# Kernel tuning notes

Measured on AMD Instinct MI355X. Metric: run time of the kernel, lower is better.

## Reference

```python
import jax, jax.numpy as jnp
import numpy as np

H = 16
D_K = 64
HALF_WINDOW = 256  # window_size // 2 = 512 // 2


def setup_inputs() -> dict:
    key = jax.random.key(0)
    ks = jax.random.split(key, 9)
    B, S, D = 2, 2048, 1024
    scale = 0.02
    return {
        "x": jax.random.normal(ks[0], (B, S, D), dtype=jnp.float32),
        "Wq": jax.random.normal(ks[1], (D, D), dtype=jnp.float32) * scale,
        "bq": jax.random.normal(ks[2], (D,), dtype=jnp.float32) * scale,
        "Wk": jax.random.normal(ks[3], (D, D), dtype=jnp.float32) * scale,
        "bk": jax.random.normal(ks[4], (D,), dtype=jnp.float32) * scale,
        "Wv": jax.random.normal(ks[5], (D, D), dtype=jnp.float32) * scale,
        "bv": jax.random.normal(ks[6], (D,), dtype=jnp.float32) * scale,
        "Wo": jax.random.normal(ks[7], (D, D), dtype=jnp.float32) * scale,
        "bo": jax.random.normal(ks[8], (D,), dtype=jnp.float32) * scale,
    }


def reference(x, Wq, bq, Wk, bk, Wv, bv, Wo, bo):
    B, S, D = x.shape
    # projections -> [B, H, S, d_k]
    q = (x @ Wq + bq).reshape(B, S, H, D_K).transpose(0, 2, 1, 3)
    k = (x @ Wk + bk).reshape(B, S, H, D_K).transpose(0, 2, 1, 3)
    v = (x @ Wv + bv).reshape(B, S, H, D_K).transpose(0, 2, 1, 3)
    # dense scores, as in the original module
    scores = jnp.einsum("bhqd,bhkd->bhqk", q, k) / jnp.sqrt(jnp.float32(D_K))
    # sliding window band mask: 0 inside |i-j| <= half_window, -inf outside
    idx = jnp.arange(S)
    band = jnp.abs(idx[:, None] - idx[None, :]) <= HALF_WINDOW  # [S, S]
    window_mask = jnp.where(band, jnp.float32(0.0), -jnp.inf)
    scores = scores + window_mask[None, None, :, :]
    attn = jax.nn.softmax(scores, axis=-1)  # dropout is identity (p=0 / eval)
    out = jnp.einsum("bhqk,bhkd->bhqd", attn, v)  # [B, H, S, d_k]
    out = out.transpose(0, 2, 1, 3).reshape(B, S, D)
    return out @ Wo + bo
```

## Files before the change

### kernel.cpp

```cpp
#include <hip/hip_runtime.h>
#include <hip/hip_bf16.h>
#include <cstdint>
#include <cstddef>

using bf16 = __hip_bfloat16;
typedef __attribute__((ext_vector_type(8))) short bf16x8v;
typedef __attribute__((ext_vector_type(4))) float f32x4v;
typedef __attribute__((ext_vector_type(16))) float f32x16v;
typedef __attribute__((ext_vector_type(4))) int i32x4v;

__device__ __forceinline__ f32x4v mfma16x16x32(bf16x8v a, bf16x8v b, f32x4v c) {
  return __builtin_amdgcn_mfma_f32_16x16x32_bf16(a, b, c, 0, 0, 0);
}
__device__ __forceinline__ f32x16v mfma32x32x16(bf16x8v a, bf16x8v b, f32x16v c) {
  return __builtin_amdgcn_mfma_f32_32x32x16_bf16(a, b, c, 0, 0, 0);
}

__device__ __forceinline__ void lds_async16(const void* g, void* l) {
  __builtin_amdgcn_global_load_lds(
      (__attribute__((address_space(1))) void*)g,
      (__attribute__((address_space(3))) void*)l, 16, 0, 0);
}

__device__ __forceinline__ unsigned short f2bf_bits(float f) {
  union { bf16 h; unsigned short u; } cv;
  cv.h = __float2bfloat16(f);
  return cv.u;
}
__device__ __forceinline__ uint32_t pk_bf2(float a, float b) {
  return (uint32_t)f2bf_bits(a) | ((uint32_t)f2bf_bits(b) << 16);
}

#define QSC 0.18033688011111793f


__global__ void convert_x_k(const float* __restrict__ x, bf16* __restrict__ xb) {
  const int i = blockIdx.x * blockDim.x + threadIdx.x;
  const float4 v = reinterpret_cast<const float4*>(x)[i];
  ushort4 o;
  o.x = f2bf_bits(v.x); o.y = f2bf_bits(v.y);
  o.z = f2bf_bits(v.z); o.w = f2bf_bits(v.w);
  reinterpret_cast<ushort4*>(xb)[i] = o;
}

__global__ void transpose_w_k(const float* __restrict__ Wq, const float* __restrict__ Wk,
                              const float* __restrict__ Wv, const float* __restrict__ Wo,
                              bf16* __restrict__ wcat, bf16* __restrict__ wot) {
  __shared__ float tile[64][65];
  const int mat = blockIdx.z;
  const float* W = (mat == 0) ? Wq : (mat == 1) ? Wk : (mat == 2) ? Wv : Wo;
  bf16* dst = (mat < 3) ? (wcat + (size_t)mat * 1024 * 1024) : wot;
  const int n0 = blockIdx.x * 64, k0 = blockIdx.y * 64;
  const int tr = threadIdx.x >> 6, tc = threadIdx.x & 63;
#pragma unroll
  for (int it = 0; it < 16; ++it)
    tile[it * 4 + tr][tc] = W[(size_t)(k0 + it * 4 + tr) * 1024 + n0 + tc];
  __syncthreads();
#pragma unroll
  for (int it = 0; it < 16; ++it) {
    const int n = n0 + it * 4 + tr;
    dst[(size_t)n * 1024 + k0 + tc] = __float2bfloat16(tile[tc][it * 4 + tr]);
  }
}

__global__ void build_bias_k(const float* __restrict__ bq, const float* __restrict__ bk,
                             const float* __restrict__ bv, float* __restrict__ bcat) {
  const int i = blockIdx.x * 256 + threadIdx.x;
  if (i < 3072)
    bcat[i] = (i < 1024) ? bq[i] : (i < 2048) ? bk[i - 1024] : bv[i - 2048];
}

template <int EPI>
__global__ __launch_bounds__(256, 3) void gemm_k(
    const bf16* __restrict__ A, const bf16* __restrict__ Bt,
    const float* __restrict__ bias,
    bf16* __restrict__ qb, bf16* __restrict__ kb, bf16* __restrict__ vtb,
    float* __restrict__ outf)
{
  constexpr int K = 1024;
  __shared__ bf16 smem[16384];
  const int t = threadIdx.x;
  const int lane = t & 63, w = t >> 6;
  const int g = lane >> 4, r = lane & 15;
  const int wr = w >> 1, wc = w & 1;
  const int m0 = blockIdx.x * 128, n0 = blockIdx.y * 128;

  const int srow = t >> 2;
  const int scol = ((lane & 3) ^ g) << 3;
  const bf16* aS0 = A + (size_t)(m0 + srow) * K + scol;
  const bf16* aS1 = A + (size_t)(m0 + 64 + srow) * K + scol;
  const bf16* bS0 = Bt + (size_t)(n0 + srow) * K + scol;
  const bf16* bS1 = Bt + (size_t)(n0 + 64 + srow) * K + scol;

  f32x4v acc[4][4] = {};

  auto STAGE = [&](int kt, int buf) {
    const int ko = kt * 32;
    char* d0 = (char*)smem + buf * 16384 + w * 1024;
    lds_async16(aS0 + ko, d0);
    lds_async16(aS1 + ko, d0 + 4096);
    lds_async16(bS0 + ko, d0 + 8192);
    lds_async16(bS1 + ko, d0 + 12288);
  };

  const int csw = (g ^ ((r >> 2) & 3)) << 4;

  STAGE(0, 0);
  asm volatile("s_waitcnt vmcnt(0)" ::: "memory");
  __builtin_amdgcn_s_barrier();

  for (int kt = 0; kt < 32; ++kt) {
    if (kt < 31) STAGE(kt + 1, (kt + 1) & 1);

    const char* buf = (const char*)smem + (kt & 1) * 16384;
    bf16x8v af[4], bfr[4];
#pragma unroll
    for (int m = 0; m < 4; ++m)
      af[m] = *reinterpret_cast<const bf16x8v*>(buf + (wr * 64 + m * 16 + r) * 64 + csw);
#pragma unroll
    for (int n = 0; n < 4; ++n)
      bfr[n] = *reinterpret_cast<const bf16x8v*>(buf + 8192 + (wc * 64 + n * 16 + r) * 64 + csw);
#pragma unroll
    for (int m = 0; m < 4; ++m)
#pragma unroll
      for (int n = 0; n < 4; ++n)
        acc[m][n] = mfma16x16x32(af[m], bfr[n], acc[m][n]);

    if (kt < 31) asm volatile("s_waitcnt vmcnt(0)" ::: "memory");
    __builtin_amdgcn_s_barrier();
  }

  if (EPI == 0) {
    const int gcol0 = n0 + wc * 64;
    const int mat = gcol0 >> 10;
    const int hh = (gcol0 & 1023) >> 6;
    const int s0 = m0 + wr * 64;
    const int b_ = s0 >> 11, sb = s0 & 2047;
    const size_t bh = (size_t)(b_ * 16 + hh);
    unsigned short* ep = (unsigned short*)smem + w * 4096;

#pragma unroll
    for (int n = 0; n < 4; ++n) {
      const int dkl = n * 16 + r;
      const float bv_ = bias[gcol0 + dkl];
#pragma unroll
      for (int m = 0; m < 4; ++m) {
#pragma unroll
        for (int v = 0; v < 4; ++v) {
          const int sl = m * 16 + g * 4 + v;
          const float val = acc[m][n][v] + bv_;
          if (mat == 0)      ep[sl * 64 + dkl] = f2bf_bits(val * QSC);
          else if (mat == 1) ep[sl * 64 + dkl] = f2bf_bits(val);
          else               ep[dkl * 64 + sl] = f2bf_bits(val);
        }
      }
    }
#pragma unroll
    for (int i = 0; i < 8; ++i) {
      const int chunk = i * 64 + lane;
      const int rw = chunk >> 3;
      const int off = (chunk & 7) * 8;
      const bf16x8v vv = *reinterpret_cast<const bf16x8v*>(ep + rw * 64 + off);
      if (mat == 0)
        *reinterpret_cast<bf16x8v*>(qb + (bh * 2048 + sb + rw) * 64 + off) = vv;
      else if (mat == 1)
        *reinterpret_cast<bf16x8v*>(kb + (bh * 2048 + sb + rw) * 64 + off) = vv;
      else
        *reinterpret_cast<bf16x8v*>(vtb + (bh * 64 + rw) * 2048 + sb + off) = vv;
    }
  } else {
#pragma unroll
    for (int n = 0; n < 4; ++n) {
      const int gcol = n0 + wc * 64 + n * 16 + r;
      const float bv_ = bias[gcol];
#pragma unroll
      for (int m = 0; m < 4; ++m) {
#pragma unroll
        for (int v = 0; v < 4; ++v) {
          const int grow = m0 + wr * 64 + m * 16 + g * 4 + v;
          outf[(size_t)grow * 1024 + gcol] = acc[m][n][v] + bv_;
        }
      }
    }
  }
}

__global__ __launch_bounds__(64) void attn_k(
    const bf16* __restrict__ qb, const bf16* __restrict__ kb_,
    const bf16* __restrict__ vtb, bf16* __restrict__ aout)
{
  constexpr int S = 2048;
  const int lane = threadIdx.x & 63;
  const int hi = lane >> 5, l31 = lane & 31;
  const int d_ = blockIdx.x;
  const int xcd = d_ & 7, slot = d_ >> 3;
  const int bh_i = xcd * 4 + (slot >> 6);
  const int q0 = (slot & 63) * 32;
  const int b = bh_i >> 4, h = bh_i & 15;
  const size_t bh = (size_t)b * 16 + h;
  const bf16* qp = qb + bh * (size_t)(S * 64);
  const bf16* kp = kb_ + bh * (size_t)(S * 64);
  const bf16* vp = vtb + bh * (size_t)(64 * S);

  bf16x8v qf[4];
#pragma unroll
  for (int i = 0; i < 4; ++i)
    qf[i] = *reinterpret_cast<const bf16x8v*>(&qp[(size_t)(q0 + l31) * 64 + i * 16 + hi * 8]);

  f32x16v o0 = {}, o1 = {};
  float lrun = 0.f;

  const int jlo = (q0 >= 256) ? (q0 - 256) : 0;
  const int jend = (q0 + 256 <= S - 32) ? (q0 + 256) : (S - 32);
  const int nIter = ((jend - jlo) >> 5) + 1;

  auto LDK = [&](int j, bf16x8v* kf) {
    const bf16* p0 = kp + (size_t)(j + l31) * 64 + hi * 8;
#pragma unroll
    for (int i = 0; i < 4; ++i)
      kf[i] = *reinterpret_cast<const bf16x8v*>(p0 + i * 16);
  };
  auto LDV = [&](int j, bf16x8v* vf) {
#pragma unroll
    for (int db = 0; db < 2; ++db)
#pragma unroll
      for (int kk = 0; kk < 2; ++kk)
        vf[db * 2 + kk] = *reinterpret_cast<const bf16x8v*>(
            &vp[(size_t)(db * 32 + l31) * S + j + kk * 16 + hi * 8]);
  };

  auto STEP = [&](int idx, bf16x8v* kc, bf16x8v* vc, bf16x8v* kn, bf16x8v* vn) {
    const int j = jlo + idx * 32;
    if (idx + 1 < nIter) { LDK(j + 32, kn); LDV(j + 32, vn); }

    f32x16v s = {};
#pragma unroll
    for (int i = 0; i < 4; ++i) s = mfma32x32x16(kc[i], qf[i], s);

    float p[16];
    const bool needMask = ((q0 + 31 - j) > 256) || ((j + 31 - q0) > 256);
    if (needMask) {
      const int base = l31 - 4 * hi + (q0 - j) + 256;
#pragma unroll
      for (int tt = 0; tt < 4; ++tt)
#pragma unroll
        for (int e = 0; e < 4; ++e) {
          const int kk_ = 8 * tt + e;
          const float ev = __builtin_amdgcn_exp2f(s[4 * tt + e]);
          p[4 * tt + e] = ((unsigned)(base - kk_) <= 512u) ? ev : 0.f;
        }
    } else {
#pragma unroll
      for (int i = 0; i < 16; ++i) p[i] = __builtin_amdgcn_exp2f(s[i]);
    }
    lrun += (((p[0] + p[1]) + (p[2] + p[3])) + ((p[4] + p[5]) + (p[6] + p[7]))) +
            (((p[8] + p[9]) + (p[10] + p[11])) + ((p[12] + p[13]) + (p[14] + p[15])));

    uint32_t W00 = pk_bf2(p[0],  p[1]),  W01 = pk_bf2(p[2],  p[3]);
    uint32_t W10 = pk_bf2(p[4],  p[5]),  W11 = pk_bf2(p[6],  p[7]);
    uint32_t W20 = pk_bf2(p[8],  p[9]),  W21 = pk_bf2(p[10], p[11]);
    uint32_t W30 = pk_bf2(p[12], p[13]), W31 = pk_bf2(p[14], p[15]);
    asm volatile("v_permlane32_swap_b32 %0, %1" : "+v"(W00), "+v"(W10));
    asm volatile("v_permlane32_swap_b32 %0, %1" : "+v"(W01), "+v"(W11));
    asm volatile("v_permlane32_swap_b32 %0, %1" : "+v"(W20), "+v"(W30));
    asm volatile("v_permlane32_swap_b32 %0, %1" : "+v"(W21), "+v"(W31));
    union { i32x4v i; bf16x8v hv; } c0, c1;
    c0.i = (i32x4v){(int)W00, (int)W01, (int)W10, (int)W11};
    c1.i = (i32x4v){(int)W20, (int)W21, (int)W30, (int)W31};
    o0 = mfma32x32x16(vc[0], c0.hv, o0);
    o0 = mfma32x32x16(vc[1], c1.hv, o0);
    o1 = mfma32x32x16(vc[2], c0.hv, o1);
    o1 = mfma32x32x16(vc[3], c1.hv, o1);
  };

  bf16x8v ka[4], va[4], kn2[4], vn2[4];
  LDK(jlo, ka); LDV(jlo, va);
  int it = 0;
  while (it + 2 <= nIter) {
    STEP(it, ka, va, kn2, vn2);
    STEP(it + 1, kn2, vn2, ka, va);
    it += 2;
  }
  if (it < nIter) STEP(it, ka, va, kn2, vn2);

  lrun += __shfl_xor(lrun, 32);
  const float inv = 1.0f / lrun;

  const size_t ob = ((size_t)b * S + q0 + l31) * 1024 + h * 64 + hi * 4;
#pragma unroll
  for (int tt = 0; tt < 4; ++tt) {
    uint2 u;
    u.x = pk_bf2(o0[4 * tt] * inv, o0[4 * tt + 1] * inv);
    u.y = pk_bf2(o0[4 * tt + 2] * inv, o0[4 * tt + 3] * inv);
    *reinterpret_cast<uint2*>(&aout[ob + 8 * tt]) = u;
    uint2 v2;
    v2.x = pk_bf2(o1[4 * tt] * inv, o1[4 * tt + 1] * inv);
    v2.y = pk_bf2(o1[4 * tt + 2] * inv, o1[4 * tt + 3] * inv);
    *reinterpret_cast<uint2*>(&aout[ob + 32 + 8 * tt]) = v2;
  }
}

extern "C" void kernel_launch(void* const* d_in, const int* in_sizes, int n_in,
                              void* d_out, int out_size, void* d_ws, size_t ws_size,
                              hipStream_t stream) {
  (void)in_sizes; (void)n_in; (void)out_size; (void)ws_size;
  const float* x  = (const float*)d_in[0];
  const float* Wq = (const float*)d_in[1];
  const float* bq = (const float*)d_in[2];
  const float* Wk = (const float*)d_in[3];
  const float* bk = (const float*)d_in[4];
  const float* Wv = (const float*)d_in[5];
  const float* bv = (const float*)d_in[6];
  const float* Wo = (const float*)d_in[7];
  const float* bo = (const float*)d_in[8];
  float* out = (float*)d_out;

  char* ws = (char*)d_ws;
  bf16*  xb    = (bf16*)(ws);
  bf16*  wcat  = (bf16*)(ws + 8388608);
  bf16*  wot   = (bf16*)(ws + 14680064);
  bf16*  qbuf  = (bf16*)(ws + 16777216);
  bf16*  kbuf  = (bf16*)(ws + 25165824);
  bf16*  vtbuf = (bf16*)(ws + 33554432);
  bf16*  aoutb = (bf16*)(ws + 41943040);
  float* bcat  = (float*)(ws + 50331648);

  convert_x_k<<<4096, 256, 0, stream>>>(x, xb);
  transpose_w_k<<<dim3(16, 16, 4), 256, 0, stream>>>(Wq, Wk, Wv, Wo, wcat, wot);
  build_bias_k<<<12, 256, 0, stream>>>(bq, bk, bv, bcat);

  gemm_k<0><<<dim3(32, 24), 256, 0, stream>>>(xb, wcat, bcat, qbuf, kbuf, vtbuf, nullptr);
  attn_k<<<2048, 64, 0, stream>>>(qbuf, kbuf, vtbuf, aoutb);
  gemm_k<1><<<dim3(32, 8), 256, 0, stream>>>(aoutb, wot, bo, nullptr, nullptr, nullptr, out);
}
```

Baseline: 105.4 us.

## Split attention key range across two waves and merge prep kernels

```diff
diff --git a/kernel.cpp b/kernel.cpp
--- a/kernel.cpp
+++ b/kernel.cpp
@@ -33,41 +33,44 @@
 
 #define QSC 0.18033688011111793f
 
-
-__global__ void convert_x_k(const float* __restrict__ x, bf16* __restrict__ xb) {
-  const int i = blockIdx.x * blockDim.x + threadIdx.x;
-  const float4 v = reinterpret_cast<const float4*>(x)[i];
-  ushort4 o;
-  o.x = f2bf_bits(v.x); o.y = f2bf_bits(v.y);
-  o.z = f2bf_bits(v.z); o.w = f2bf_bits(v.w);
-  reinterpret_cast<ushort4*>(xb)[i] = o;
-}
-
-__global__ void transpose_w_k(const float* __restrict__ Wq, const float* __restrict__ Wk,
-                              const float* __restrict__ Wv, const float* __restrict__ Wo,
-                              bf16* __restrict__ wcat, bf16* __restrict__ wot) {
+__global__ void prep_k(const float* __restrict__ x,
+                       const float* __restrict__ Wq, const float* __restrict__ Wk,
+                       const float* __restrict__ Wv, const float* __restrict__ Wo,
+                       const float* __restrict__ bq, const float* __restrict__ bk,
+                       const float* __restrict__ bv,
+                       bf16* __restrict__ xb, bf16* __restrict__ wcat,
+                       bf16* __restrict__ wot, float* __restrict__ bcat)
+{
   __shared__ float tile[64][65];
-  const int mat = blockIdx.z;
-  const float* W = (mat == 0) ? Wq : (mat == 1) ? Wk : (mat == 2) ? Wv : Wo;
-  bf16* dst = (mat < 3) ? (wcat + (size_t)mat * 1024 * 1024) : wot;
-  const int n0 = blockIdx.x * 64, k0 = blockIdx.y * 64;
-  const int tr = threadIdx.x >> 6, tc = threadIdx.x & 63;
-#pragma unroll
-  for (int it = 0; it < 16; ++it)
-    tile[it * 4 + tr][tc] = W[(size_t)(k0 + it * 4 + tr) * 1024 + n0 + tc];
-  __syncthreads();
-#pragma unroll
-  for (int it = 0; it < 16; ++it) {
-    const int n = n0 + it * 4 + tr;
-    dst[(size_t)n * 1024 + k0 + tc] = __float2bfloat16(tile[tc][it * 4 + tr]);
-  }
-}
-
-__global__ void build_bias_k(const float* __restrict__ bq, const float* __restrict__ bk,
-                             const float* __restrict__ bv, float* __restrict__ bcat) {
-  const int i = blockIdx.x * 256 + threadIdx.x;
-  if (i < 3072)
-    bcat[i] = (i < 1024) ? bq[i] : (i < 2048) ? bk[i - 1024] : bv[i - 2048];
+  const int bid = blockIdx.x;
+  if (bid < 4096) {
+    const int i = bid * 256 + threadIdx.x;
+    const float4 v = reinterpret_cast<const float4*>(x)[i];
+    ushort4 o;
+    o.x = f2bf_bits(v.x); o.y = f2bf_bits(v.y);
+    o.z = f2bf_bits(v.z); o.w = f2bf_bits(v.w);
+    reinterpret_cast<ushort4*>(xb)[i] = o;
+  } else if (bid < 5120) {
+    const int b2 = bid - 4096;
+    const int mat = b2 >> 8;
+    const float* W = (mat == 0) ? Wq : (mat == 1) ? Wk : (mat == 2) ? Wv : Wo;
+    bf16* dst = (mat < 3) ? (wcat + (size_t)mat * 1024 * 1024) : wot;
+    const int n0 = ((b2 >> 4) & 15) * 64, k0 = (b2 & 15) * 64;
+    const int tr = threadIdx.x >> 6, tc = threadIdx.x & 63;
+#pragma unroll
+    for (int it = 0; it < 16; ++it)
+      tile[it * 4 + tr][tc] = W[(size_t)(k0 + it * 4 + tr) * 1024 + n0 + tc];
+    __syncthreads();
+#pragma unroll
+    for (int it = 0; it < 16; ++it) {
+      const int n = n0 + it * 4 + tr;
+      dst[(size_t)n * 1024 + k0 + tc] = __float2bfloat16(tile[tc][it * 4 + tr]);
+    }
+  } else {
+    const int i = (bid - 5120) * 256 + threadIdx.x;
+    if (i < 3072)
+      bcat[i] = (i < 1024) ? bq[i] : (i < 2048) ? bk[i - 1024] : bv[i - 2048];
+  }
 }
 
 template <int EPI>
@@ -185,12 +188,14 @@
   }
 }
 
-__global__ __launch_bounds__(64) void attn_k(
+__global__ __launch_bounds__(128) void attn_k(
     const bf16* __restrict__ qb, const bf16* __restrict__ kb_,
     const bf16* __restrict__ vtb, bf16* __restrict__ aout)
 {
   constexpr int S = 2048;
-  const int lane = threadIdx.x & 63;
+  const int tid = threadIdx.x;
+  const int wid = tid >> 6;
+  const int lane = tid & 63;
   const int hi = lane >> 5, l31 = lane & 31;
   const int d_ = blockIdx.x;
   const int xcd = d_ & 7, slot = d_ >> 3;
@@ -202,6 +207,8 @@
   const bf16* kp = kb_ + bh * (size_t)(S * 64);
   const bf16* vp = vtb + bh * (size_t)(64 * S);
 
+  __shared__ float msum[64 * 33];
+
   bf16x8v qf[4];
 #pragma unroll
   for (int i = 0; i < 4; ++i)
@@ -213,6 +220,9 @@
   const int jlo = (q0 >= 256) ? (q0 - 256) : 0;
   const int jend = (q0 + 256 <= S - 32) ? (q0 + 256) : (S - 32);
   const int nIter = ((jend - jlo) >> 5) + 1;
+  const int h_ = (nIter + 1) >> 1;
+  const int myN = wid ? (nIter - h_) : h_;
+  const int jlo_w = jlo + (wid ? h_ * 32 : 0);
 
   auto LDK = [&](int j, bf16x8v* kf) {
     const bf16* p0 = kp + (size_t)(j + l31) * 64 + hi * 8;
@@ -230,8 +240,8 @@
   };
 
   auto STEP = [&](int idx, bf16x8v* kc, bf16x8v* vc, bf16x8v* kn, bf16x8v* vn) {
-    const int j = jlo + idx * 32;
-    if (idx + 1 < nIter) { LDK(j + 32, kn); LDV(j + 32, vn); }
+    const int j = jlo_w + idx * 32;
+    if (idx + 1 < myN) { LDK(j + 32, kn); LDV(j + 32, vn); }
 
     f32x16v s = {};
 #pragma unroll
@@ -274,29 +284,42 @@
   };
 
   bf16x8v ka[4], va[4], kn2[4], vn2[4];
-  LDK(jlo, ka); LDV(jlo, va);
+  LDK(jlo_w, ka); LDV(jlo_w, va);
   int it = 0;
-  while (it + 2 <= nIter) {
+  while (it + 2 <= myN) {
     STEP(it, ka, va, kn2, vn2);
     STEP(it + 1, kn2, vn2, ka, va);
     it += 2;
   }
-  if (it < nIter) STEP(it, ka, va, kn2, vn2);
-
-  lrun += __shfl_xor(lrun, 32);
-  const float inv = 1.0f / lrun;
-
-  const size_t ob = ((size_t)b * S + q0 + l31) * 1024 + h * 64 + hi * 4;
-#pragma unroll
-  for (int tt = 0; tt < 4; ++tt) {
-    uint2 u;
-    u.x = pk_bf2(o0[4 * tt] * inv, o0[4 * tt + 1] * inv);
-    u.y = pk_bf2(o0[4 * tt + 2] * inv, o0[4 * tt + 3] * inv);
-    *reinterpret_cast<uint2*>(&aout[ob + 8 * tt]) = u;
-    uint2 v2;
-    v2.x = pk_bf2(o1[4 * tt] * inv, o1[4 * tt + 1] * inv);
-    v2.y = pk_bf2(o1[4 * tt + 2] * inv, o1[4 * tt + 3] * inv);
-    *reinterpret_cast<uint2*>(&aout[ob + 32 + 8 * tt]) = v2;
+  if (it < myN) STEP(it, ka, va, kn2, vn2);
+
+  if (wid == 1) {
+    float* mp = msum + lane * 33;
+#pragma unroll
+    for (int i = 0; i < 16; ++i) { mp[i] = o0[i]; mp[16 + i] = o1[i]; }
+    mp[32] = lrun;
+  }
+  __syncthreads();
+  if (wid == 0) {
+    const float* mp = msum + lane * 33;
+#pragma unroll
+    for (int i = 0; i < 16; ++i) { o0[i] += mp[i]; o1[i] += mp[16 + i]; }
+    lrun += mp[32];
+    lrun += __shfl_xor(lrun, 32);
+    const float inv = 1.0f / lrun;
+
+    const size_t ob = ((size_t)b * S + q0 + l31) * 1024 + h * 64 + hi * 4;
+#pragma unroll
+    for (int tt = 0; tt < 4; ++tt) {
+      uint2 u;
+      u.x = pk_bf2(o0[4 * tt] * inv, o0[4 * tt + 1] * inv);
+      u.y = pk_bf2(o0[4 * tt + 2] * inv, o0[4 * tt + 3] * inv);
+      *reinterpret_cast<uint2*>(&aout[ob + 8 * tt]) = u;
+      uint2 v2;
+      v2.x = pk_bf2(o1[4 * tt] * inv, o1[4 * tt + 1] * inv);
+      v2.y = pk_bf2(o1[4 * tt + 2] * inv, o1[4 * tt + 3] * inv);
+      *reinterpret_cast<uint2*>(&aout[ob + 32 + 8 * tt]) = v2;
+    }
   }
 }
 
@@ -325,11 +348,10 @@
   bf16*  aoutb = (bf16*)(ws + 41943040);
   float* bcat  = (float*)(ws + 50331648);
 
-  convert_x_k<<<4096, 256, 0, stream>>>(x, xb);
-  transpose_w_k<<<dim3(16, 16, 4), 256, 0, stream>>>(Wq, Wk, Wv, Wo, wcat, wot);
-  build_bias_k<<<12, 256, 0, stream>>>(bq, bk, bv, bcat);
+  prep_k<<<5132, 256, 0, stream>>>(x, Wq, Wk, Wv, Wo, bq, bk, bv,
+                                   xb, wcat, wot, bcat);
 
   gemm_k<0><<<dim3(32, 24), 256, 0, stream>>>(xb, wcat, bcat, qbuf, kbuf, vtbuf, nullptr);
-  attn_k<<<2048, 64, 0, stream>>>(qbuf, kbuf, vtbuf, aoutb);
+  attn_k<<<2048, 128, 0, stream>>>(qbuf, kbuf, vtbuf, aoutb);
   gemm_k<1><<<dim3(32, 8), 256, 0, stream>>>(aoutb, wot, bo, nullptr, nullptr, nullptr, out);
 }
```

New measurement: 102.0 us. 3.2% less time.
